# Kernel optimization log

Hardware: AMD Instinct MI355X
Metric: run time of the kernel (lower is better)

The kernel has to match this reference:

```python
import jax, jax.numpy as jnp
import numpy as np

N, E, F_IN = 100000, 1000000, 128
H, C = 4, 32
HC = H * C
D_DIR = 128
G = 250
HID, CLS = 128, 2
ALPHA = 0.5
NEG = 0.2  # LeakyReLU slope in GATv2


def setup_inputs() -> dict:
    key = jax.random.key(0)
    ks = jax.random.split(key, 16)
    p = lambda k, shape: 0.02 * jax.random.normal(k, shape, jnp.float32)
    return {
        "x": jax.random.normal(ks[0], (N, F_IN), jnp.float32),
        "edge_index": jax.random.randint(ks[1], (2, E), 0, N, dtype=jnp.int32),
        "edge_attr": jax.random.normal(ks[2], (E, 1), jnp.float32),
        "batch": jnp.sort(jax.random.randint(ks[3], (N,), 0, G, dtype=jnp.int32)),
        "dir_w_in": p(ks[4], (2, F_IN, D_DIR)),
        "dir_b_in": jnp.zeros((2, D_DIR), jnp.float32),
        "dir_w_out": p(ks[5], (2, F_IN, D_DIR)),
        "dir_b_out": jnp.zeros((2, D_DIR), jnp.float32),
        "gat_wl": p(ks[6], (F_IN, HC)),
        "gat_wr": p(ks[7], (F_IN, HC)),
        "gat_we": p(ks[8], (1, HC)),
        "gat_att": p(ks[9], (H, C)),
        "gat_b": jnp.zeros((HC,), jnp.float32),
        "w1": p(ks[10], (D_DIR + HC, HID)),
        "b1": jnp.zeros((HID,), jnp.float32),
        "w2": p(ks[11], (HID, CLS)),
        "b2": jnp.zeros((CLS,), jnp.float32),
    }


def _gcn(x, src, dst, W, b):
    # GCNConv with add_self_loops=False (forced by DirGNNConv), unit edge weights.
    deg = jnp.zeros((N,), x.dtype).at[dst].add(1.0)
    dinv = jnp.where(deg > 0, 1.0 / jnp.sqrt(jnp.maximum(deg, 1.0)), 0.0)
    norm = dinv[src] * dinv[dst]  # [E]
    h = x @ W  # [N, D]
    out = jnp.zeros((N, W.shape[1]), x.dtype).at[dst].add(norm[:, None] * h[src])
    return out + b


def _mean_pool(h, batch):
    cnt = jnp.zeros((G,), h.dtype).at[batch].add(1.0)
    s = jnp.zeros((G, h.shape[1]), h.dtype).at[batch].add(h)
    return s / jnp.maximum(cnt, 1.0)[:, None]


def _forward(x, edge_index, edge_attr, batch, dir_w_in, dir_b_in, dir_w_out, dir_b_out,
             gat_wl, gat_wr, gat_we, gat_att, gat_b, w1, b1, w2, b2):
    src, dst = edge_index[0], edge_index[1]
    # --- DirGNN branch: alpha * GCN(flipped edges) + (1-alpha) * GCN(edges), relu between ---
    h = x
    for i in range(2):
        x_in = _gcn(h, src, dst, dir_w_in[i], dir_b_in[i])
        x_out = _gcn(h, dst, src, dir_w_out[i], dir_b_out[i])
        h = jax.nn.relu(ALPHA * x_out + (1.0 - ALPHA) * x_in)
    x1 = _mean_pool(h, batch)  # [G, D_DIR]
    # --- GATv2 branch (self loops appended, edge_attr fill value 1.0) ---
    loop = jnp.arange(N, dtype=src.dtype)
    s2 = jnp.concatenate([src, loop])
    d2 = jnp.concatenate([dst, loop])
    ea = jnp.concatenate([edge_attr, jnp.ones((N, 1), edge_attr.dtype)], axis=0)
    gl = (x @ gat_wl).reshape(N, H, C)  # source transform
    gr = (x @ gat_wr).reshape(N, H, C)  # target transform
    ee = (ea @ gat_we).reshape(-1, H, C)
    e = jax.nn.leaky_relu(gl[s2] + gr[d2] + ee, NEG)  # [E+N, H, C]
    logits = jnp.einsum('ehc,hc->eh', e, gat_att)
    # segment softmax over incoming edges of each target node (self loops => nonempty)
    m = jnp.full((N, H), -jnp.inf, logits.dtype).at[d2].max(logits)
    ex = jnp.exp(logits - m[d2])
    denom = jnp.zeros((N, H), logits.dtype).at[d2].add(ex)
    att = ex / denom[d2]
    out2 = jnp.zeros((N, H, C), x.dtype).at[d2].add(att[:, :, None] * gl[s2])
    x2 = _mean_pool(out2.reshape(N, HC) + gat_b, batch)  # [G, HC]
    # --- head ---
    z = jnp.concatenate([x1, x2], axis=1)
    z = jax.nn.relu(z @ w1 + b1)
    return z @ w2 + b2  # [G, CLS]


def reference(x, edge_index, edge_attr, batch, dir_w_in, dir_b_in, dir_w_out, dir_b_out,
              gat_wl, gat_wr, gat_we, gat_att, gat_b, w1, b1, w2, b2):
    return _forward(x, edge_index, edge_attr, batch, dir_w_in, dir_b_in, dir_w_out, dir_b_out,
                    gat_wl, gat_wr, gat_we, gat_att, gat_b, w1, b1, w2, b2)
```

## Files before the change

### kernel.cpp

```cpp
#include <hip/hip_runtime.h>
#include <cstdint>

#define FDIM 128
#define PCH 64

static inline int cdiv(long long a, long long b) { return (int)((a + b - 1) / b); }

__global__ __launch_bounds__(256) void degi_kernel(const int* __restrict__ src,
                                                   const int* __restrict__ dst,
                                                   int* __restrict__ deg_in,
                                                   int* __restrict__ deg_out, int E) {
  int base = (blockIdx.x * 256 + threadIdx.x) * 4;
  if (base + 4 <= E) {
    int4 s4 = *(const int4*)(src + base);
    int4 d4 = *(const int4*)(dst + base);
    atomicAdd(&deg_in[d4.x], 1);
    atomicAdd(&deg_in[d4.y], 1);
    atomicAdd(&deg_in[d4.z], 1);
    atomicAdd(&deg_in[d4.w], 1);
    atomicAdd(&deg_out[s4.x], 1);
    atomicAdd(&deg_out[s4.y], 1);
    atomicAdd(&deg_out[s4.z], 1);
    atomicAdd(&deg_out[s4.w], 1);
  } else {
    for (int i = base; i < E; i++) {
      atomicAdd(&deg_in[dst[i]], 1);
      atomicAdd(&deg_out[src[i]], 1);
    }
  }
}

__global__ __launch_bounds__(256) void dinv2_kernel(const int* __restrict__ degs,
                                                    float* __restrict__ dinv, int n2) {
  int i = blockIdx.x * 256 + threadIdx.x;
  if (i < n2) {
    int v = degs[i];
    dinv[i] = v > 0 ? 1.0f / sqrtf((float)v) : 0.f;
  }
}

__global__ __launch_bounds__(256) void cnt_sorted(const int* __restrict__ batch,
                                                  float* __restrict__ cnt, int N, int G) {
  int g = blockIdx.x * 256 + threadIdx.x;
  if (g >= G) return;
  int lo = 0, hi = N;
  while (lo < hi) { int mid = (lo + hi) >> 1; if (batch[mid] < g) lo = mid + 1; else hi = mid; }
  int lo2 = lo, hi2 = N;
  while (lo2 < hi2) { int mid = (lo2 + hi2) >> 1; if (batch[mid] <= g) lo2 = mid + 1; else hi2 = mid; }
  cnt[g] = (float)(lo2 - lo);
}

__global__ __launch_bounds__(256) void scan1(const int* __restrict__ in, int* __restrict__ out,
                                             int* __restrict__ bsums, int n) {
  __shared__ int tmp[256];
  int t = threadIdx.x;
  int base = blockIdx.x * 1024 + t * 4;
  int a[4];
#pragma unroll
  for (int j = 0; j < 4; j++) a[j] = (base + j < n) ? in[base + j] : 0;
  int s = a[0] + a[1] + a[2] + a[3];
  tmp[t] = s;
  __syncthreads();
  for (int off = 1; off < 256; off <<= 1) {
    int v = (t >= off) ? tmp[t - off] : 0;
    __syncthreads();
    tmp[t] += v;
    __syncthreads();
  }
  int excl = tmp[t] - s;
  int run = excl;
#pragma unroll
  for (int j = 0; j < 4; j++) {
    if (base + j < n) out[base + j] = run;
    run += a[j];
  }
  if (t == 255) bsums[blockIdx.x] = tmp[255];
}

__global__ __launch_bounds__(256) void scan2(const int* __restrict__ bsums,
                                             int* __restrict__ boff, int nb) {
  __shared__ int tmp[256];
  int t = threadIdx.x;
  int s = (t < nb) ? bsums[t] : 0;
  tmp[t] = s;
  __syncthreads();
  for (int off = 1; off < 256; off <<= 1) {
    int v = (t >= off) ? tmp[t - off] : 0;
    __syncthreads();
    tmp[t] += v;
    __syncthreads();
  }
  if (t < nb) boff[t] = tmp[t] - s;
}

__global__ __launch_bounds__(256) void scan3(int* __restrict__ out, const int* __restrict__ boff,
                                             int* __restrict__ cur, int n) {
  int i = blockIdx.x * 256 + threadIdx.x;
  if (i < n) {
    int v = out[i] + boff[i >> 10];
    out[i] = v;
    cur[i] = v;
  }
}

__global__ __launch_bounds__(256) void fill_kernel(const int* __restrict__ src,
                                                   const int* __restrict__ dst,
                                                   const float* __restrict__ eattr,
                                                   int* __restrict__ cur_in,
                                                   int* __restrict__ cur_out,
                                                   int2* __restrict__ csr_in,
                                                   int* __restrict__ csr_out_dst, int E) {
  int base = (blockIdx.x * 256 + threadIdx.x) * 4;
  if (base + 4 <= E) {
    int4 s4 = *(const int4*)(src + base);
    int4 d4 = *(const int4*)(dst + base);
    float4 e4 = *(const float4*)(eattr + base);
    int p0 = atomicAdd(&cur_in[d4.x], 1);
    int p1 = atomicAdd(&cur_in[d4.y], 1);
    int p2 = atomicAdd(&cur_in[d4.z], 1);
    int p3 = atomicAdd(&cur_in[d4.w], 1);
    int q0 = atomicAdd(&cur_out[s4.x], 1);
    int q1 = atomicAdd(&cur_out[s4.y], 1);
    int q2 = atomicAdd(&cur_out[s4.z], 1);
    int q3 = atomicAdd(&cur_out[s4.w], 1);
    csr_in[p0] = make_int2(s4.x, __float_as_int(e4.x));
    csr_in[p1] = make_int2(s4.y, __float_as_int(e4.y));
    csr_in[p2] = make_int2(s4.z, __float_as_int(e4.z));
    csr_in[p3] = make_int2(s4.w, __float_as_int(e4.w));
    csr_out_dst[q0] = d4.x;
    csr_out_dst[q1] = d4.y;
    csr_out_dst[q2] = d4.z;
    csr_out_dst[q3] = d4.w;
  } else {
    for (int i = base; i < E; i++) {
      int s = src[i], d = dst[i];
      int p = atomicAdd(&cur_in[d], 1);
      csr_in[p] = make_int2(s, __float_as_int(eattr[i]));
      int q = atomicAdd(&cur_out[s], 1);
      csr_out_dst[q] = d;
    }
  }
}

__global__ __launch_bounds__(256) void mm128d(const float* __restrict__ A,
                                              const float* __restrict__ W0,
                                              const float* __restrict__ W1,
                                              float* __restrict__ out0,
                                              float* __restrict__ out1, int nrows) {
  __shared__ float As[64][128];
  __shared__ float Ws[128][64];
  int r0 = blockIdx.x * 64;
  int tid = threadIdx.x;

#pragma unroll
  for (int i = 0; i < 8; i++) {
    int v = tid + 256 * i;
    int r = v >> 5, k4 = (v & 31) << 2;
    int row = r0 + r;
    float4 a;
    if (row < nrows) a = *(const float4*)(A + (size_t)row * FDIM + k4);
    else a = make_float4(0.f, 0.f, 0.f, 0.f);
    int swz = ((r >> 2) & 7) << 2;
    *(float4*)(&As[r][k4 ^ swz]) = a;
  }

  int tx = tid & 15, ty = tid >> 4;
  int rbase = ty * 4;
  int swz = (ty & 7) << 2;

  for (int wsel = 0; wsel < 2; wsel++) {
    const float* W = wsel ? W1 : W0;
    float* out = wsel ? out1 : out0;
#pragma unroll
    for (int half = 0; half < 2; half++) {
      __syncthreads();
      int cb = half * 64;
#pragma unroll
      for (int i = 0; i < 8; i++) {
        int v = tid + 256 * i;
        int k = v >> 4, c4 = (v & 15) << 2;
        *(float4*)(&Ws[k][c4]) = *(const float4*)(W + k * FDIM + cb + c4);
      }
      __syncthreads();

      float acc[4][4] = {};
#pragma unroll 8
      for (int k = 0; k < 128; k++) {
        int kx = k ^ swz;
        float a0 = As[rbase + 0][kx];
        float a1 = As[rbase + 1][kx];
        float a2 = As[rbase + 2][kx];
        float a3 = As[rbase + 3][kx];
        float4 w = *(float4*)(&Ws[k][tx * 4]);
        acc[0][0] += a0 * w.x; acc[0][1] += a0 * w.y; acc[0][2] += a0 * w.z; acc[0][3] += a0 * w.w;
        acc[1][0] += a1 * w.x; acc[1][1] += a1 * w.y; acc[1][2] += a1 * w.z; acc[1][3] += a1 * w.w;
        acc[2][0] += a2 * w.x; acc[2][1] += a2 * w.y; acc[2][2] += a2 * w.z; acc[2][3] += a2 * w.w;
        acc[3][0] += a3 * w.x; acc[3][1] += a3 * w.y; acc[3][2] += a3 * w.z; acc[3][3] += a3 * w.w;
      }
#pragma unroll
      for (int rr = 0; rr < 4; rr++) {
        int row = r0 + rbase + rr;
        if (row < nrows) {
          float4 o = make_float4(acc[rr][0], acc[rr][1], acc[rr][2], acc[rr][3]);
          *(float4*)(out + (size_t)row * FDIM + cb + tx * 4) = o;
        }
      }
    }
  }
}

__global__ __launch_bounds__(128) void gcn_gather4(const float4* __restrict__ tin,
                                                   const float4* __restrict__ tout,
                                                   const int* __restrict__ rp_in,
                                                   const int* __restrict__ deg_in,
                                                   const int2* __restrict__ adj_in,
                                                   const int* __restrict__ rp_out,
                                                   const int* __restrict__ deg_out,
                                                   const int* __restrict__ adj_out,
                                                   const float* __restrict__ dinv_in,
                                                   const float* __restrict__ dinv_out,
                                                   const float* __restrict__ bin,
                                                   const float* __restrict__ bout,
                                                   float4* __restrict__ outp, int N) {
  int grp = threadIdx.x >> 5, lane = threadIdx.x & 31;
  int d = blockIdx.x * 4 + grp;
  if (d >= N) return;
  float wi = 0.5f * dinv_in[d], wo = 0.5f * dinv_out[d];
  float4 a0 = make_float4(0.f, 0.f, 0.f, 0.f);
  float4 a1 = a0, a2 = a0, a3 = a0;

  int p = rp_in[d], n1 = deg_in[d];
  int k = 0;
  for (; k + 4 <= n1; k += 4) {
    int s0 = adj_in[p + k].x, s1 = adj_in[p + k + 1].x, s2 = adj_in[p + k + 2].x, s3 = adj_in[p + k + 3].x;
    float w0 = wi * dinv_in[s0], w1 = wi * dinv_in[s1], w2 = wi * dinv_in[s2], w3 = wi * dinv_in[s3];
    float4 v0 = tin[(size_t)s0 * 32 + lane];
    float4 v1 = tin[(size_t)s1 * 32 + lane];
    float4 v2 = tin[(size_t)s2 * 32 + lane];
    float4 v3 = tin[(size_t)s3 * 32 + lane];
    a0.x += w0 * v0.x; a0.y += w0 * v0.y; a0.z += w0 * v0.z; a0.w += w0 * v0.w;
    a1.x += w1 * v1.x; a1.y += w1 * v1.y; a1.z += w1 * v1.z; a1.w += w1 * v1.w;
    a2.x += w2 * v2.x; a2.y += w2 * v2.y; a2.z += w2 * v2.z; a2.w += w2 * v2.w;
    a3.x += w3 * v3.x; a3.y += w3 * v3.y; a3.z += w3 * v3.z; a3.w += w3 * v3.w;
  }
  for (; k < n1; k++) {
    int s = adj_in[p + k].x;
    float w = wi * dinv_in[s];
    float4 v = tin[(size_t)s * 32 + lane];
    a0.x += w * v.x; a0.y += w * v.y; a0.z += w * v.z; a0.w += w * v.w;
  }

  int q = rp_out[d], n2 = deg_out[d];
  k = 0;
  for (; k + 4 <= n2; k += 4) {
    int s0 = adj_out[q + k], s1 = adj_out[q + k + 1], s2 = adj_out[q + k + 2], s3 = adj_out[q + k + 3];
    float w0 = wo * dinv_out[s0], w1 = wo * dinv_out[s1], w2 = wo * dinv_out[s2], w3 = wo * dinv_out[s3];
    float4 v0 = tout[(size_t)s0 * 32 + lane];
    float4 v1 = tout[(size_t)s1 * 32 + lane];
    float4 v2 = tout[(size_t)s2 * 32 + lane];
    float4 v3 = tout[(size_t)s3 * 32 + lane];
    a0.x += w0 * v0.x; a0.y += w0 * v0.y; a0.z += w0 * v0.z; a0.w += w0 * v0.w;
    a1.x += w1 * v1.x; a1.y += w1 * v1.y; a1.z += w1 * v1.z; a1.w += w1 * v1.w;
    a2.x += w2 * v2.x; a2.y += w2 * v2.y; a2.z += w2 * v2.z; a2.w += w2 * v2.w;
    a3.x += w3 * v3.x; a3.y += w3 * v3.y; a3.z += w3 * v3.z; a3.w += w3 * v3.w;
  }
  for (; k < n2; k++) {
    int s = adj_out[q + k];
    float w = wo * dinv_out[s];
    float4 v = tout[(size_t)s * 32 + lane];
    a0.x += w * v.x; a0.y += w * v.y; a0.z += w * v.z; a0.w += w * v.w;
  }

  float4 acc;
  acc.x = (a0.x + a1.x) + (a2.x + a3.x);
  acc.y = (a0.y + a1.y) + (a2.y + a3.y);
  acc.z = (a0.z + a1.z) + (a2.z + a3.z);
  acc.w = (a0.w + a1.w) + (a2.w + a3.w);

  const float4* b1 = (const float4*)bin;
  const float4* b2 = (const float4*)bout;
  float4 ba = b1[lane], bb = b2[lane];
  float4 o;
  o.x = acc.x + 0.5f * (ba.x + bb.x);
  o.y = acc.y + 0.5f * (ba.y + bb.y);
  o.z = acc.z + 0.5f * (ba.z + bb.z);
  o.w = acc.w + 0.5f * (ba.w + bb.w);
  o.x = o.x > 0.f ? o.x : 0.f;
  o.y = o.y > 0.f ? o.y : 0.f;
  o.z = o.z > 0.f ? o.z : 0.f;
  o.w = o.w > 0.f ? o.w : 0.f;
  outp[(size_t)d * 32 + lane] = o;
}

__global__ __launch_bounds__(128) void gat_fused2(const float4* __restrict__ gl,
                                                  const float4* __restrict__ gr,
                                                  const int* __restrict__ rp,
                                                  const int* __restrict__ deg,
                                                  const int2* __restrict__ adj,
                                                  const float* __restrict__ we,
                                                  const float* __restrict__ att,
                                                  const float* __restrict__ gatb,
                                                  float4* __restrict__ outp, int N) {
  int grp = threadIdx.x >> 5, lane = threadIdx.x & 31;
  int d = blockIdx.x * 4 + grp;
  if (d >= N) return;

  float4 grv = gr[(size_t)d * 32 + lane];
  float4 wev = ((const float4*)we)[lane];
  float4 atv = ((const float4*)att)[lane];

  int p = rp[d], n1 = deg[d];
  float m = -1e30f, den = 0.f;
  float4 o = make_float4(0.f, 0.f, 0.f, 0.f);

#define GAT_LOGIT(g4, ea, pv)                                                     \
  {                                                                               \
    float vx = g4.x + grv.x + (ea) * wev.x; vx = vx > 0.f ? vx : 0.2f * vx;       \
    float vy = g4.y + grv.y + (ea) * wev.y; vy = vy > 0.f ? vy : 0.2f * vy;       \
    float vz = g4.z + grv.z + (ea) * wev.z; vz = vz > 0.f ? vz : 0.2f * vz;       \
    float vw = g4.w + grv.w + (ea) * wev.w; vw = vw > 0.f ? vw : 0.2f * vw;       \
    pv = vx * atv.x + vy * atv.y + vz * atv.z + vw * atv.w;                       \
    pv += __shfl_xor(pv, 1);                                                      \
    pv += __shfl_xor(pv, 2);                                                      \
    pv += __shfl_xor(pv, 4);                                                      \
  }

#define GAT_UPDATE(g4, pv)                                                        \
  {                                                                               \
    float mn = fmaxf(m, pv);                                                      \
    float sc = expf(m - mn);                                                      \
    float w = expf(pv - mn);                                                      \
    den = den * sc + w;                                                           \
    o.x = o.x * sc + w * g4.x;                                                    \
    o.y = o.y * sc + w * g4.y;                                                    \
    o.z = o.z * sc + w * g4.z;                                                    \
    o.w = o.w * sc + w * g4.w;                                                    \
    m = mn;                                                                       \
  }

  int k = 0;
  for (; k + 2 <= n1; k += 2) {
    int2 e0 = adj[p + k], e1 = adj[p + k + 1];
    int s0 = e0.x, s1 = e1.x;
    float ea0 = __int_as_float(e0.y), ea1 = __int_as_float(e1.y);
    float4 g0 = gl[(size_t)s0 * 32 + lane];
    float4 g1 = gl[(size_t)s1 * 32 + lane];
    float pv0, pv1;
    GAT_LOGIT(g0, ea0, pv0);
    GAT_LOGIT(g1, ea1, pv1);
    GAT_UPDATE(g0, pv0);
    GAT_UPDATE(g1, pv1);
  }
  if (k < n1) {
    int2 e = adj[p + k];
    float ea = __int_as_float(e.y);
    float4 g = gl[(size_t)e.x * 32 + lane];
    float pv;
    GAT_LOGIT(g, ea, pv);
    GAT_UPDATE(g, pv);
  }
  {
    float4 g = gl[(size_t)d * 32 + lane];
    float pv;
    GAT_LOGIT(g, 1.0f, pv);
    GAT_UPDATE(g, pv);
  }
#undef GAT_LOGIT
#undef GAT_UPDATE

  float4 bb = ((const float4*)gatb)[lane];
  float4 r;
  r.x = o.x / den + bb.x;
  r.y = o.y / den + bb.y;
  r.z = o.z / den + bb.z;
  r.w = o.w / den + bb.w;
  outp[(size_t)d * 32 + lane] = r;
}

__global__ __launch_bounds__(128) void pool_kernel(const float* __restrict__ srcf,
                                                   const int* __restrict__ batch,
                                                   float* __restrict__ zb,
                                                   int colOff, int N) {
  __shared__ int sb[PCH];
  int c0 = blockIdx.x * PCH;
  int t = threadIdx.x;
  int nmax = N - c0; if (nmax > PCH) nmax = PCH;
  if (t < nmax) sb[t] = batch[c0 + t];
  __syncthreads();
  float run = 0.f;
  int gp = sb[0];
  for (int i = 0; i < nmax; i++) {
    int g = sb[i];
    if (g != gp) {
      atomicAdd(&zb[(size_t)gp * 256 + colOff + t], run);
      run = 0.f; gp = g;
    }
    run += srcf[(size_t)(c0 + i) * FDIM + t];
  }
  atomicAdd(&zb[(size_t)gp * 256 + colOff + t], run);
}

__global__ __launch_bounds__(128) void head_kernel(const float* __restrict__ zb,
                                                   const float* __restrict__ cnt,
                                                   const float* __restrict__ w1,
                                                   const float* __restrict__ b1,
                                                   const float* __restrict__ w2,
                                                   const float* __restrict__ b2,
                                                   float* __restrict__ out, int G) {
  __shared__ float z[256];
  __shared__ float y[128];
  int g = blockIdx.x, t = threadIdx.x;
  float c = cnt[g];
  float cm = c > 1.f ? c : 1.f;
  z[t]       = zb[(size_t)g * 256 + t] / cm;
  z[t + 128] = zb[(size_t)g * 256 + 128 + t] / cm;
  __syncthreads();
  float acc = b1[t];
  for (int k = 0; k < 256; k++) acc += z[k] * w1[k * 128 + t];
  y[t] = acc > 0.f ? acc : 0.f;
  __syncthreads();
  if (t < 2) {
    float o = b2[t];
    for (int j = 0; j < 128; j++) o += y[j] * w2[j * 2 + t];
    out[(size_t)g * 2 + t] = o;
  }
}

extern "C" void kernel_launch(void* const* d_in, const int* in_sizes, int n_in,
                              void* d_out, int out_size, void* d_ws, size_t ws_size,
                              hipStream_t stream) {
  const float* x     = (const float*)d_in[0];
  const int*   ei    = (const int*)d_in[1];
  const float* eattr = (const float*)d_in[2];
  const int*   batch = (const int*)d_in[3];
  const float* dwi   = (const float*)d_in[4];
  const float* dbi   = (const float*)d_in[5];
  const float* dwo   = (const float*)d_in[6];
  const float* dbo   = (const float*)d_in[7];
  const float* wl    = (const float*)d_in[8];
  const float* wr    = (const float*)d_in[9];
  const float* we    = (const float*)d_in[10];
  const float* att   = (const float*)d_in[11];
  const float* gatb  = (const float*)d_in[12];
  const float* w1    = (const float*)d_in[13];
  const float* b1    = (const float*)d_in[14];
  const float* w2    = (const float*)d_in[15];
  const float* b2    = (const float*)d_in[16];

  int N = in_sizes[0] / FDIM;
  int E = in_sizes[1] / 2;
  int G = out_size / 2;
  const int* src = ei;
  const int* dst = ei + E;

  float* ws = (float*)d_ws;
  size_t off = 0;
  float* A        = ws + off; off += (size_t)N * FDIM;
  float* B        = ws + off; off += (size_t)N * FDIM;
  float* C        = ws + off; off += (size_t)N * FDIM;
  float* dinv2    = ws + off; off += 2 * (size_t)N;
  int* deg2       = (int*)(ws + off); off += 2 * (size_t)N;
  int* rp_in      = (int*)(ws + off); off += (size_t)N;
  int* rp_out     = (int*)(ws + off); off += (size_t)N;
  int* cur_in     = (int*)(ws + off); off += (size_t)N;
  int* cur_out    = (int*)(ws + off); off += (size_t)N;
  int2* csr_in    = (int2*)(ws + off); off += 2 * (size_t)E;
  int* csr_out_dst= (int*)(ws + off); off += (size_t)E;
  int* bsums      = (int*)(ws + off); off += 256;
  int* boff       = (int*)(ws + off); off += 256;
  float* zb       = ws + off; off += (size_t)G * 256;
  float* cnt      = ws + off; off += (size_t)G;

  int* deg_in = deg2, *deg_out = deg2 + N;
  float* dinv_in = dinv2, *dinv_out = dinv2 + N;

  int nb1 = cdiv(N, 1024);

  hipMemsetAsync(deg2, 0, 2 * (size_t)N * sizeof(int), stream);
  degi_kernel<<<cdiv(E, 1024), 256, 0, stream>>>(src, dst, deg_in, deg_out, E);
  dinv2_kernel<<<cdiv(2LL * N, 256), 256, 0, stream>>>(deg2, dinv2, 2 * N);
  scan1<<<nb1, 256, 0, stream>>>(deg_in, rp_in, bsums, N);
  scan2<<<1, 256, 0, stream>>>(bsums, boff, nb1);
  scan3<<<cdiv(N, 256), 256, 0, stream>>>(rp_in, boff, cur_in, N);
  scan1<<<nb1, 256, 0, stream>>>(deg_out, rp_out, bsums, N);
  scan2<<<1, 256, 0, stream>>>(bsums, boff, nb1);
  scan3<<<cdiv(N, 256), 256, 0, stream>>>(rp_out, boff, cur_out, N);
  fill_kernel<<<cdiv(E, 1024), 256, 0, stream>>>(src, dst, eattr, cur_in, cur_out,
                                                 csr_in, csr_out_dst, E);

  hipMemsetAsync(zb, 0, (size_t)G * 256 * sizeof(float), stream);
  cnt_sorted<<<cdiv(G, 256), 256, 0, stream>>>(batch, cnt, N, G);

  mm128d<<<cdiv(N, 64), 256, 0, stream>>>(x, dwi, dwo, B, C, N);
  gcn_gather4<<<cdiv(N, 4), 128, 0, stream>>>((const float4*)B, (const float4*)C,
                                              rp_in, deg_in, csr_in,
                                              rp_out, deg_out, csr_out_dst,
                                              dinv_in, dinv_out, dbi, dbo, (float4*)A, N);
  mm128d<<<cdiv(N, 64), 256, 0, stream>>>(A, dwi + 16384, dwo + 16384, B, C, N);
  gcn_gather4<<<cdiv(N, 4), 128, 0, stream>>>((const float4*)B, (const float4*)C,
                                              rp_in, deg_in, csr_in,
                                              rp_out, deg_out, csr_out_dst,
                                              dinv_in, dinv_out, dbi + 128, dbo + 128, (float4*)A, N);
  pool_kernel<<<cdiv(N, PCH), 128, 0, stream>>>(A, batch, zb, 0, N);

  mm128d<<<cdiv(N, 64), 256, 0, stream>>>(x, wl, wr, B, C, N);
  gat_fused2<<<cdiv(N, 4), 128, 0, stream>>>((const float4*)B, (const float4*)C,
                                             rp_in, deg_in, csr_in,
                                             we, att, gatb, (float4*)A, N);
  pool_kernel<<<cdiv(N, PCH), 128, 0, stream>>>(A, batch, zb, 128, N);

  head_kernel<<<G, 128, 0, stream>>>(zb, cnt, w1, b1, w2, b2, (float*)d_out, G);
}
```

Baseline: 1.207 ms.

## Merge in/out degree scans, halve per-thread edges, prefetch weights in GEMM

The two separate exclusive scans over in- and out-degrees become one scan over the concatenated 2N array, with scan3 splitting the result and subtracting E for the out half. This removes three kernel launches. The degree and CSR fill kernels now handle 2 edges per thread instead of 4, doubling the grid for more parallelism in the atomic-heavy passes. The mm128d GEMM now register-prefetches the next 64-column weight tile while computing the current one, hiding global load latency at the cost of extra registers.

```diff
diff --git a/kernel.cpp b/kernel.cpp
--- a/kernel.cpp
+++ b/kernel.cpp
@@ -10,18 +10,14 @@
                                                    const int* __restrict__ dst,
                                                    int* __restrict__ deg_in,
                                                    int* __restrict__ deg_out, int E) {
-  int base = (blockIdx.x * 256 + threadIdx.x) * 4;
-  if (base + 4 <= E) {
-    int4 s4 = *(const int4*)(src + base);
-    int4 d4 = *(const int4*)(dst + base);
-    atomicAdd(&deg_in[d4.x], 1);
-    atomicAdd(&deg_in[d4.y], 1);
-    atomicAdd(&deg_in[d4.z], 1);
-    atomicAdd(&deg_in[d4.w], 1);
-    atomicAdd(&deg_out[s4.x], 1);
-    atomicAdd(&deg_out[s4.y], 1);
-    atomicAdd(&deg_out[s4.z], 1);
-    atomicAdd(&deg_out[s4.w], 1);
+  int base = (blockIdx.x * 256 + threadIdx.x) * 2;
+  if (base + 2 <= E) {
+    int2 s2 = *(const int2*)(src + base);
+    int2 d2 = *(const int2*)(dst + base);
+    atomicAdd(&deg_in[d2.x], 1);
+    atomicAdd(&deg_in[d2.y], 1);
+    atomicAdd(&deg_out[s2.x], 1);
+    atomicAdd(&deg_out[s2.y], 1);
   } else {
     for (int i = base; i < E; i++) {
       atomicAdd(&deg_in[dst[i]], 1);
@@ -93,13 +89,16 @@
   if (t < nb) boff[t] = tmp[t] - s;
 }
 
-__global__ __launch_bounds__(256) void scan3(int* __restrict__ out, const int* __restrict__ boff,
-                                             int* __restrict__ cur, int n) {
+__global__ __launch_bounds__(256) void scan3(const int* __restrict__ scanned,
+                                             const int* __restrict__ boff,
+                                             int* __restrict__ rp_in, int* __restrict__ cur_in,
+                                             int* __restrict__ rp_out, int* __restrict__ cur_out,
+                                             int N, int E, int n2) {
   int i = blockIdx.x * 256 + threadIdx.x;
-  if (i < n) {
-    int v = out[i] + boff[i >> 10];
-    out[i] = v;
-    cur[i] = v;
+  if (i < n2) {
+    int v = scanned[i] + boff[i >> 10];
+    if (i < N) { rp_in[i] = v; cur_in[i] = v; }
+    else { v -= E; rp_out[i - N] = v; cur_out[i - N] = v; }
   }
 }
 
@@ -110,27 +109,19 @@
                                                    int* __restrict__ cur_out,
                                                    int2* __restrict__ csr_in,
                                                    int* __restrict__ csr_out_dst, int E) {
-  int base = (blockIdx.x * 256 + threadIdx.x) * 4;
-  if (base + 4 <= E) {
-    int4 s4 = *(const int4*)(src + base);
-    int4 d4 = *(const int4*)(dst + base);
-    float4 e4 = *(const float4*)(eattr + base);
-    int p0 = atomicAdd(&cur_in[d4.x], 1);
-    int p1 = atomicAdd(&cur_in[d4.y], 1);
-    int p2 = atomicAdd(&cur_in[d4.z], 1);
-    int p3 = atomicAdd(&cur_in[d4.w], 1);
-    int q0 = atomicAdd(&cur_out[s4.x], 1);
-    int q1 = atomicAdd(&cur_out[s4.y], 1);
-    int q2 = atomicAdd(&cur_out[s4.z], 1);
-    int q3 = atomicAdd(&cur_out[s4.w], 1);
-    csr_in[p0] = make_int2(s4.x, __float_as_int(e4.x));
-    csr_in[p1] = make_int2(s4.y, __float_as_int(e4.y));
-    csr_in[p2] = make_int2(s4.z, __float_as_int(e4.z));
-    csr_in[p3] = make_int2(s4.w, __float_as_int(e4.w));
-    csr_out_dst[q0] = d4.x;
-    csr_out_dst[q1] = d4.y;
-    csr_out_dst[q2] = d4.z;
-    csr_out_dst[q3] = d4.w;
+  int base = (blockIdx.x * 256 + threadIdx.x) * 2;
+  if (base + 2 <= E) {
+    int2 s2 = *(const int2*)(src + base);
+    int2 d2 = *(const int2*)(dst + base);
+    float2 e2 = *(const float2*)(eattr + base);
+    int p0 = atomicAdd(&cur_in[d2.x], 1);
+    int p1 = atomicAdd(&cur_in[d2.y], 1);
+    int q0 = atomicAdd(&cur_out[s2.x], 1);
+    int q1 = atomicAdd(&cur_out[s2.y], 1);
+    csr_in[p0] = make_int2(s2.x, __float_as_int(e2.x));
+    csr_in[p1] = make_int2(s2.y, __float_as_int(e2.y));
+    csr_out_dst[q0] = d2.x;
+    csr_out_dst[q1] = d2.y;
   } else {
     for (int i = base; i < E; i++) {
       int s = src[i], d = dst[i];
@@ -168,42 +159,55 @@
   int rbase = ty * 4;
   int swz = (ty & 7) << 2;
 
-  for (int wsel = 0; wsel < 2; wsel++) {
-    const float* W = wsel ? W1 : W0;
-    float* out = wsel ? out1 : out0;
-#pragma unroll
-    for (int half = 0; half < 2; half++) {
-      __syncthreads();
-      int cb = half * 64;
-#pragma unroll
-      for (int i = 0; i < 8; i++) {
-        int v = tid + 256 * i;
-        int k = v >> 4, c4 = (v & 15) << 2;
-        *(float4*)(&Ws[k][c4]) = *(const float4*)(W + k * FDIM + cb + c4);
-      }
-      __syncthreads();
-
-      float acc[4][4] = {};
+  int wk[8], wc[8];
+#pragma unroll
+  for (int i = 0; i < 8; i++) {
+    int v = tid + 256 * i;
+    wk[i] = v >> 4; wc[i] = (v & 15) << 2;
+  }
+
+  float4 wreg[8];
+#pragma unroll
+  for (int i = 0; i < 8; i++)
+    wreg[i] = *(const float4*)(W0 + wk[i] * FDIM + wc[i]);
+
+  for (int p = 0; p < 4; p++) {
+    const float* Wn = (p < 1) ? (W0 + 64) : (p < 2) ? W1 : (W1 + 64);
+    float* out = (p < 2) ? out0 : out1;
+    int cb = (p & 1) * 64;
+
+    __syncthreads();
+#pragma unroll
+    for (int i = 0; i < 8; i++)
+      *(float4*)(&Ws[wk[i]][wc[i]]) = wreg[i];
+    __syncthreads();
+
+    if (p < 3) {
+#pragma unroll
+      for (int i = 0; i < 8; i++)
+        wreg[i] = *(const float4*)(Wn + wk[i] * FDIM + wc[i]);
+    }
+
+    float acc[4][4] = {};
 #pragma unroll 8
-      for (int k = 0; k < 128; k++) {
-        int kx = k ^ swz;
-        float a0 = As[rbase + 0][kx];
-        float a1 = As[rbase + 1][kx];
-        float a2 = As[rbase + 2][kx];
-        float a3 = As[rbase + 3][kx];
-        float4 w = *(float4*)(&Ws[k][tx * 4]);
-        acc[0][0] += a0 * w.x; acc[0][1] += a0 * w.y; acc[0][2] += a0 * w.z; acc[0][3] += a0 * w.w;
-        acc[1][0] += a1 * w.x; acc[1][1] += a1 * w.y; acc[1][2] += a1 * w.z; acc[1][3] += a1 * w.w;
-        acc[2][0] += a2 * w.x; acc[2][1] += a2 * w.y; acc[2][2] += a2 * w.z; acc[2][3] += a2 * w.w;
-        acc[3][0] += a3 * w.x; acc[3][1] += a3 * w.y; acc[3][2] += a3 * w.z; acc[3][3] += a3 * w.w;
-      }
-#pragma unroll
-      for (int rr = 0; rr < 4; rr++) {
-        int row = r0 + rbase + rr;
-        if (row < nrows) {
-          float4 o = make_float4(acc[rr][0], acc[rr][1], acc[rr][2], acc[rr][3]);
-          *(float4*)(out + (size_t)row * FDIM + cb + tx * 4) = o;
-        }
+    for (int k = 0; k < 128; k++) {
+      int kx = k ^ swz;
+      float a0 = As[rbase + 0][kx];
+      float a1 = As[rbase + 1][kx];
+      float a2 = As[rbase + 2][kx];
+      float a3 = As[rbase + 3][kx];
+      float4 w = *(float4*)(&Ws[k][tx * 4]);
+      acc[0][0] += a0 * w.x; acc[0][1] += a0 * w.y; acc[0][2] += a0 * w.z; acc[0][3] += a0 * w.w;
+      acc[1][0] += a1 * w.x; acc[1][1] += a1 * w.y; acc[1][2] += a1 * w.z; acc[1][3] += a1 * w.w;
+      acc[2][0] += a2 * w.x; acc[2][1] += a2 * w.y; acc[2][2] += a2 * w.z; acc[2][3] += a2 * w.w;
+      acc[3][0] += a3 * w.x; acc[3][1] += a3 * w.y; acc[3][2] += a3 * w.z; acc[3][3] += a3 * w.w;
+    }
+#pragma unroll
+    for (int rr = 0; rr < 4; rr++) {
+      int row = r0 + rbase + rr;
+      if (row < nrows) {
+        float4 o = make_float4(acc[rr][0], acc[rr][1], acc[rr][2], acc[rr][3]);
+        *(float4*)(out + (size_t)row * FDIM + cb + tx * 4) = o;
       }
     }
   }
@@ -460,6 +464,7 @@
   float* C        = ws + off; off += (size_t)N * FDIM;
   float* dinv2    = ws + off; off += 2 * (size_t)N;
   int* deg2       = (int*)(ws + off); off += 2 * (size_t)N;
+  int* rpt        = (int*)(ws + off); off += 2 * (size_t)N;
   int* rp_in      = (int*)(ws + off); off += (size_t)N;
   int* rp_out     = (int*)(ws + off); off += (size_t)N;
   int* cur_in     = (int*)(ws + off); off += (size_t)N;
@@ -474,19 +479,17 @@
   int* deg_in = deg2, *deg_out = deg2 + N;
   float* dinv_in = dinv2, *dinv_out = dinv2 + N;
 
-  int nb1 = cdiv(N, 1024);
-
-  hipMemsetAsync(deg2, 0, 2 * (size_t)N * sizeof(int), stream);
-  degi_kernel<<<cdiv(E, 1024), 256, 0, stream>>>(src, dst, deg_in, deg_out, E);
-  dinv2_kernel<<<cdiv(2LL * N, 256), 256, 0, stream>>>(deg2, dinv2, 2 * N);
-  scan1<<<nb1, 256, 0, stream>>>(deg_in, rp_in, bsums, N);
+  int n2 = 2 * N;
+  int nb1 = cdiv(n2, 1024);
+
+  hipMemsetAsync(deg2, 0, (size_t)n2 * sizeof(int), stream);
+  degi_kernel<<<cdiv(E, 512), 256, 0, stream>>>(src, dst, deg_in, deg_out, E);
+  dinv2_kernel<<<cdiv((long long)n2, 256), 256, 0, stream>>>(deg2, dinv2, n2);
+  scan1<<<nb1, 256, 0, stream>>>(deg2, rpt, bsums, n2);
   scan2<<<1, 256, 0, stream>>>(bsums, boff, nb1);
-  scan3<<<cdiv(N, 256), 256, 0, stream>>>(rp_in, boff, cur_in, N);
-  scan1<<<nb1, 256, 0, stream>>>(deg_out, rp_out, bsums, N);
-  scan2<<<1, 256, 0, stream>>>(bsums, boff, nb1);
-  scan3<<<cdiv(N, 256), 256, 0, stream>>>(rp_out, boff, cur_out, N);
-  fill_kernel<<<cdiv(E, 1024), 256, 0, stream>>>(src, dst, eattr, cur_in, cur_out,
-                                                 csr_in, csr_out_dst, E);
+  scan3<<<cdiv(n2, 256), 256, 0, stream>>>(rpt, boff, rp_in, cur_in, rp_out, cur_out, N, E, n2);
+  fill_kernel<<<cdiv(E, 512), 256, 0, stream>>>(src, dst, eattr, cur_in, cur_out,
+                                                csr_in, csr_out_dst, E);
 
   hipMemsetAsync(zb, 0, (size_t)G * 256 * sizeof(float), stream);
   cnt_sorted<<<cdiv(G, 256), 256, 0, stream>>>(batch, cnt, N, G);
```

New measurement: 1.289 ms. +6.8%, slower.
